# Optimization experiments

Hardware: AMD Instinct MI355X
Metric: run time of the kernel (lower is better)

The kernel has to match this reference:

```python
import jax, jax.numpy as jnp
import numpy as np

# ---- constants mirroring ATSSPostProcessor defaults / metainfo ----
PRE_NMS_THRESH = 0.05
PRE_NMS_TOP_N = 1000
NMS_THRESH = 0.6
POST_TOP_N = 100
IMG_H, IMG_W = 800.0, 1216.0      # metainfo img_shape
BW_XY, BW_WH = 10.0, 5.0          # GLIP/ATSS box coder weights (10,10,5,5)
MAX_DWH = float(np.log(1000.0 / 16.0))
CLASS_OFFSET = 10000.0            # batched_nms class offset (> max coord)


def setup_inputs() -> dict:
    key = jax.random.key(0)
    k0, k1, k2, k3 = jax.random.split(key, 4)
    N, C, L, H, W = 8, 80, 256, 100, 152
    box_regression = jax.random.normal(k0, (N, 4, H, W), jnp.float32)
    centerness = jax.random.normal(k1, (N, 1, H, W), jnp.float32)
    box_cls = jax.random.normal(k2, (N, C, H, W), jnp.float32)
    dot_product_logits = jax.random.normal(k3, (N, H * W, L), jnp.float32)
    # stride-8 grid anchors with base size 64
    ys, xs = np.meshgrid(np.arange(H), np.arange(W), indexing='ij')
    cx, cy = (xs + 0.5) * 8.0, (ys + 0.5) * 8.0
    anchors = jnp.asarray(
        np.stack([cx - 32, cy - 32, cx + 32, cy + 32], -1).reshape(-1, 4),
        jnp.float32)
    # MEAN aggregation positive map: class j <- tokens [3j, 3j+1, 3j+2]
    pm = np.zeros((C, L), np.float32)
    for j in range(C):
        pm[j, 3 * j:3 * j + 3] = 1.0 / 3.0
    pos_map = jnp.asarray(pm)
    return dict(box_regression=box_regression, centerness=centerness,
                box_cls=box_cls, dot_product_logits=dot_product_logits,
                anchors=anchors, pos_map=pos_map)


def _decode(a, r):
    # delta_xywh decode with weights (10,10,5,5), clamped to img_shape
    aw, ah = a[..., 2] - a[..., 0], a[..., 3] - a[..., 1]
    acx, acy = a[..., 0] + 0.5 * aw, a[..., 1] + 0.5 * ah
    dx, dy = r[..., 0] / BW_XY, r[..., 1] / BW_XY
    dw = jnp.minimum(r[..., 2] / BW_WH, MAX_DWH)
    dh = jnp.minimum(r[..., 3] / BW_WH, MAX_DWH)
    pcx, pcy = dx * aw + acx, dy * ah + acy
    pw, ph = jnp.exp(dw) * aw, jnp.exp(dh) * ah
    x1 = jnp.clip(pcx - 0.5 * pw, 0.0, IMG_W)
    y1 = jnp.clip(pcy - 0.5 * ph, 0.0, IMG_H)
    x2 = jnp.clip(pcx + 0.5 * pw, 0.0, IMG_W)
    y2 = jnp.clip(pcy + 0.5 * ph, 0.0, IMG_H)
    return jnp.stack([x1, y1, x2, y2], -1)


def _iou_matrix(b):  # b: [K,4]
    area = (b[:, 2] - b[:, 0]) * (b[:, 3] - b[:, 1])
    ix1 = jnp.maximum(b[:, None, 0], b[None, :, 0])
    iy1 = jnp.maximum(b[:, None, 1], b[None, :, 1])
    ix2 = jnp.minimum(b[:, None, 2], b[None, :, 2])
    iy2 = jnp.minimum(b[:, None, 3], b[None, :, 3])
    inter = jnp.maximum(ix2 - ix1, 0.0) * jnp.maximum(iy2 - iy1, 0.0)
    return inter / (area[:, None] + area[None, :] - inter + 1e-6)


def _nms_single(boxes, scores, labels, valid):
    # class-aware greedy NMS (batched_nms) on fixed-size K candidates
    K = boxes.shape[0]
    s = jnp.where(valid, scores, -1.0)
    order = jnp.argsort(-s)
    b, s, l, v = boxes[order], s[order], labels[order], valid[order]
    ob = b + (l.astype(b.dtype) * CLASS_OFFSET)[:, None]
    iou = _iou_matrix(ob)
    ar = jnp.arange(K)

    def body(i, keep):
        sup = keep[i] & (iou[i] > NMS_THRESH) & (ar > i)
        return keep & ~sup

    keep = jax.lax.fori_loop(0, K, body, v)
    s2 = jnp.where(keep, s, -1.0)
    topv, topi = jax.lax.top_k(s2, POST_TOP_N)
    good = topv > 0.0
    fb = jnp.where(good[:, None], b[topi], 0.0)
    fs = jnp.where(good, topv, 0.0)
    fl = jnp.where(good, l[topi], 0)
    return fb, fs, fl


def reference(box_regression, centerness, box_cls, dot_product_logits,
              anchors, pos_map):
    N = box_regression.shape[0]
    C = pos_map.shape[0]
    HW = anchors.shape[0]
    # permute_and_flatten: [N,4,H,W] -> [N,HW,4]
    reg = box_regression.transpose(0, 2, 3, 1).reshape(N, HW, 4)
    ctr = jax.nn.sigmoid(centerness.reshape(N, HW))
    # sigmoid score fusion + MEAN grounding->od aggregation
    dp = jax.nn.sigmoid(dot_product_logits)            # [N,HW,L]
    scores = jnp.einsum('nkl,cl->nkc', dp, pos_map)    # [N,HW,C]
    cand = scores > PRE_NMS_THRESH
    fused = scores * ctr[:, :, None]
    # dynamic per-image topk over candidates == fixed-K masked top_k
    masked = jnp.where(cand, fused, -1.0).reshape(N, HW * C)
    vals, idx = jax.lax.top_k(masked, PRE_NMS_TOP_N)   # [N,K]
    valid = jnp.take_along_axis(cand.reshape(N, -1), idx, axis=1)
    loc = idx // C
    labels = idx % C + 1
    a = anchors[loc]                                           # [N,K,4]
    r = jnp.take_along_axis(reg, loc[..., None], axis=1)       # [N,K,4]
    boxes = _decode(a, r)
    sc = jnp.sqrt(jnp.maximum(vals, 0.0))
    w = boxes[..., 2] - boxes[..., 0]
    h = boxes[..., 3] - boxes[..., 1]
    valid = valid & (w > 0) & (h > 0)  # min_size = 0 filter
    # scale_factor = 1.0 -> boxes unchanged
    out_boxes, out_scores, out_labels = jax.vmap(_nms_single)(
        boxes, sc, labels, valid)
    return out_boxes, out_scores, out_labels
```

## Files before the change

### kernel.cpp

```cpp
#include <hip/hip_runtime.h>
#include <hip/hip_bf16.h>

#define NIMG 8
#define NC   80
#define NL   256
#define HWQ  15200
#define TOPK 1000
#define CAP  4096
#define SSORT 2048
#define NPOST 100
#define PERIMG (HWQ * NC)
#define TOTAL (NIMG * PERIMG)
#define NROW 16
#define NBLK (NIMG * HWQ / NROW)
#define PI4  (PERIMG / 4)
#define WPI  (PI4 / 64)
#define NWAVE (NIMG * WPI)
#define CBLK (TOTAL / 4 / 256)

__device__ __forceinline__ unsigned flipKey(float f) {
    unsigned u = __float_as_uint(f);
    return u ^ (((unsigned)((int)u >> 31)) | 0x80000000u);
}
__device__ __forceinline__ float unflipKey(unsigned k) {
    unsigned u = k ^ ((k & 0x80000000u) ? 0x80000000u : 0xFFFFFFFFu);
    return __uint_as_float(u);
}
__device__ __forceinline__ float sigmoidf(float x) {
    return 1.0f / (1.0f + expf(-x));
}

__global__ void kprep(const float* __restrict__ pm, unsigned* nnz,
                      unsigned* tok, float* wt) {
    int c = blockIdx.x * blockDim.x + threadIdx.x;
    if (c >= NC) return;
    int cnt = 0;
    for (int l = 0; l < NL; ++l) {
        float v = pm[c * NL + l];
        if (v != 0.0f) { tok[cnt * NC + c] = l; wt[cnt * NC + c] = v; cnt++; }
    }
    nnz[c] = cnt;
}

__global__ void __launch_bounds__(256)
kscoreh(const float* __restrict__ dp, const float* __restrict__ cent,
        const unsigned* __restrict__ nnz, const unsigned* __restrict__ tok,
        const float* __restrict__ wt, float* __restrict__ scores,
        unsigned* __restrict__ gh) {
    __shared__ float srow[NROW * NL];
    __shared__ unsigned h[4096];
    int t = threadIdx.x;
    for (int i = t; i < 4096; i += 256) h[i] = 0;
    long long base = (long long)blockIdx.x * NROW;
    const float4* src = (const float4*)(dp + base * NL);
    float4* dst = (float4*)srow;
#pragma unroll
    for (int j = 0; j < 4; ++j) dst[t + j * 256] = src[t + j * 256];
    __syncthreads();
    long long obase = base * NC;
#pragma unroll
    for (int j = 0; j < 5; ++j) {
        int o = t + j * 256;
        int r = o / NC, c = o - r * NC;
        const float* row = srow + r * NL;
        int m = (int)nnz[c];
        float acc = 0.0f;
        if (m == 3) {
            int t0 = (int)tok[c], t1 = (int)tok[NC + c], t2 = (int)tok[2 * NC + c];
            float w0 = wt[c], w1 = wt[NC + c], w2 = wt[2 * NC + c];
            float s0 = sigmoidf(row[t0]);
            float s1 = sigmoidf(row[t1]);
            float s2 = sigmoidf(row[t2]);
            acc += s0 * w0; acc += s1 * w1; acc += s2 * w2;
        } else {
            for (int q = 0; q < m; ++q)
                acc += sigmoidf(row[tok[q * NC + c]]) * wt[q * NC + c];
        }
        float ctr = sigmoidf(cent[base + r]);
        float sc = (acc > 0.05f) ? acc * ctr : -1.0f;
        scores[obase + o] = sc;
        atomicAdd(&h[flipKey(sc) >> 20], 1u);
    }
    __syncthreads();
    int n = (int)(base / HWQ);
    for (int i = t; i < 4096; i += 256)
        if (h[i]) atomicAdd(&gh[n * 4096 + i], h[i]);
}

__global__ void kfind1(const unsigned* __restrict__ gh, unsigned* meta) {
    __shared__ unsigned h[4096];
    __shared__ unsigned psum[256];
    int n = blockIdx.x;
    for (int i = threadIdx.x; i < 4096; i += 256) h[i] = gh[n * 4096 + i];
    __syncthreads();
    unsigned s = 0;
    for (int i = 0; i < 16; ++i) s += h[threadIdx.x * 16 + i];
    psum[threadIdx.x] = s;
    __syncthreads();
    if (threadIdx.x == 0) {
        unsigned cum = 0, above = 0; int B = 0; bool done = false;
        for (int seg = 255; seg >= 0 && !done; --seg) {
            if (cum + psum[seg] >= TOPK) {
                for (int b = seg * 16 + 15; b >= seg * 16; --b) {
                    if (cum + h[b] >= TOPK) { B = b; above = cum; done = true; break; }
                    cum += h[b];
                }
            } else cum += psum[seg];
        }
        meta[n] = (unsigned)B;
        meta[8 + n] = above;
    }
}

__global__ void __launch_bounds__(256)
kcount(const float4* __restrict__ scores4, const unsigned* __restrict__ meta,
       unsigned* __restrict__ wavecnt) {
    int i4 = blockIdx.x * 256 + threadIdx.x;
    int n = i4 / PI4;
    unsigned B = meta[n];
    float4 v = scores4[i4];
    int ns = 0;
    ns += ((flipKey(v.x) >> 20) >= B);
    ns += ((flipKey(v.y) >> 20) >= B);
    ns += ((flipKey(v.z) >> 20) >= B);
    ns += ((flipKey(v.w) >> 20) >= B);
    int s = ns;
#pragma unroll
    for (int off = 1; off < 64; off <<= 1) s += __shfl_xor(s, off);
    if ((threadIdx.x & 63) == 0) wavecnt[i4 >> 6] = (unsigned)s;
}

__global__ void __launch_bounds__(1024)
kscan(const unsigned* __restrict__ wavecnt, unsigned* __restrict__ waveoff,
      unsigned* __restrict__ cnt) {
    __shared__ unsigned ps[1024];
    int n = blockIdx.x, t = threadIdx.x;
    const unsigned* wc = wavecnt + n * WPI;
    unsigned* wo = waveoff + n * WPI;
    int s0 = t * 5;
    unsigned loc[5]; unsigned sum = 0;
#pragma unroll
    for (int j = 0; j < 5; ++j) {
        int i = s0 + j;
        unsigned vv = (i < WPI) ? wc[i] : 0u;
        loc[j] = sum; sum += vv;
    }
    ps[t] = sum;
    __syncthreads();
    for (int off = 1; off < 1024; off <<= 1) {
        unsigned add = (t >= off) ? ps[t - off] : 0u;
        __syncthreads();
        ps[t] += add;
        __syncthreads();
    }
    unsigned excl = (t > 0) ? ps[t - 1] : 0u;
#pragma unroll
    for (int j = 0; j < 5; ++j) {
        int i = s0 + j;
        if (i < WPI) wo[i] = excl + loc[j];
    }
    if (t == 1023) cnt[n] = ps[1023];
}

__global__ void __launch_bounds__(256)
kwrite(const float4* __restrict__ scores4, const unsigned* __restrict__ meta,
       const unsigned* __restrict__ waveoff, unsigned long long* __restrict__ cand) {
    int i4 = blockIdx.x * 256 + threadIdx.x;
    int n = i4 / PI4;
    unsigned B = meta[n];
    float4 v = scores4[i4];
    int li0 = (i4 - n * PI4) * 4;
    unsigned keys[4]; int sel[4]; int ns = 0;
    keys[0] = flipKey(v.x); sel[0] = (keys[0] >> 20) >= B; ns += sel[0];
    keys[1] = flipKey(v.y); sel[1] = (keys[1] >> 20) >= B; ns += sel[1];
    keys[2] = flipKey(v.z); sel[2] = (keys[2] >> 20) >= B; ns += sel[2];
    keys[3] = flipKey(v.w); sel[3] = (keys[3] >> 20) >= B; ns += sel[3];
    int lane = threadIdx.x & 63;
    int pre = ns;
#pragma unroll
    for (int off = 1; off < 64; off <<= 1) {
        int o = __shfl_up(pre, off);
        if (lane >= off) pre += o;
    }
    unsigned base = waveoff[i4 >> 6] + (unsigned)(pre - ns);
    unsigned long long* cbase = cand + (size_t)n * CAP;
#pragma unroll
    for (int e = 0; e < 4; ++e) {
        if (sel[e]) {
            if (base < CAP)
                cbase[base] = ((unsigned long long)keys[e] << 32)
                              | (unsigned)(~(li0 + e));
            base++;
        }
    }
}

__global__ void __launch_bounds__(1024)
kfine(const unsigned long long* __restrict__ cand, const unsigned* __restrict__ cnt,
      const unsigned* __restrict__ meta, unsigned long long* __restrict__ sorted) {
    __shared__ unsigned h[4096];
    __shared__ unsigned long long sbuf[SSORT];
    __shared__ unsigned psum[256];
    __shared__ unsigned selcnt;
    __shared__ unsigned Fbin;
    int n = blockIdx.x, t = threadIdx.x;
    int M = min(cnt[n], (unsigned)CAP);
    unsigned B = meta[n], above = meta[8 + n];
    const unsigned long long* cb = cand + (size_t)n * CAP;
    for (int i = t; i < 4096; i += 1024) h[i] = 0;
    sbuf[t] = 0ULL; sbuf[t + 1024] = 0ULL;
    if (t == 0) selcnt = 0;
    __syncthreads();
    for (int i = t; i < M; i += 1024) {
        unsigned key = (unsigned)(cb[i] >> 32);
        if ((key >> 20) == B) atomicAdd(&h[(key >> 8) & 0xFFFu], 1u);
    }
    __syncthreads();
    if (t < 256) {
        unsigned s = 0;
        for (int i = 0; i < 16; ++i) s += h[t * 16 + i];
        psum[t] = s;
    }
    __syncthreads();
    if (t == 0) {
        unsigned cum = above; int F = 0; bool done = false;
        for (int seg = 255; seg >= 0 && !done; --seg) {
            if (cum + psum[seg] >= TOPK) {
                for (int b = seg * 16 + 15; b >= seg * 16; --b) {
                    if (cum + h[b] >= TOPK) { F = b; done = true; break; }
                    cum += h[b];
                }
            } else cum += psum[seg];
        }
        Fbin = (unsigned)F;
    }
    __syncthreads();
    unsigned T24 = (B << 12) | Fbin;
    for (int i = t; i < M; i += 1024) {
        unsigned long long e = cb[i];
        unsigned key = (unsigned)(e >> 32);
        if ((key >> 8) >= T24) {
            unsigned p = atomicAdd(&selcnt, 1u);
            if (p < SSORT) sbuf[p] = e;
        }
    }
    __syncthreads();
    int s = (int)selcnt;
    int SN = (s <= 1024) ? 1024 : SSORT;
    for (int k = 2; k <= SN; k <<= 1) {
        for (int j = k >> 1; j > 0; j >>= 1) {
            for (int i = t; i < SN; i += 1024) {
                int l = i ^ j;
                if (l > i) {
                    unsigned long long a = sbuf[i], b = sbuf[l];
                    bool sw = ((i & k) == 0) ? (a < b) : (a > b);
                    if (sw) { sbuf[i] = b; sbuf[l] = a; }
                }
            }
            __syncthreads();
        }
    }
    if (t < TOPK) sorted[(n << 10) + t] = sbuf[t];
}

__global__ void __launch_bounds__(256)
kdecode(const unsigned long long* __restrict__ sorted,
        const float* __restrict__ anchors, const float* __restrict__ breg,
        float4* __restrict__ box4, float4* __restrict__ obx4,
        float* __restrict__ areag, unsigned* __restrict__ lblkeep) {
    int gid = blockIdx.x * 256 + threadIdx.x;
    if (gid >= NIMG * TOPK) return;
    int n = gid / TOPK, r = gid - n * TOPK;
    int o = (n << 10) + r;
    unsigned long long e = sorted[o];
    unsigned key = (unsigned)(e >> 32);
    bool real = key > 0x80000000u;
    unsigned li = ~(unsigned)(e & 0xFFFFFFFFu);
    unsigned k = li / NC, c = li - k * NC;
    int label = (int)c + 1;
    float x1 = 0, y1 = 0, x2 = 0, y2 = 0;
    bool val = false;
    if (real) {
        float a0 = anchors[k * 4 + 0], a1 = anchors[k * 4 + 1];
        float a2 = anchors[k * 4 + 2], a3 = anchors[k * 4 + 3];
        float r0 = breg[(n * 4 + 0) * HWQ + k];
        float r1 = breg[(n * 4 + 1) * HWQ + k];
        float r2 = breg[(n * 4 + 2) * HWQ + k];
        float r3 = breg[(n * 4 + 3) * HWQ + k];
        float aw = a2 - a0, ah = a3 - a1;
        float acx = a0 + 0.5f * aw, acy = a1 + 0.5f * ah;
        float dx = r0 / 10.0f, dy = r1 / 10.0f;
        float dw = fminf(r2 / 5.0f, 4.135166556742356f);
        float dh = fminf(r3 / 5.0f, 4.135166556742356f);
        float pcx = dx * aw + acx, pcy = dy * ah + acy;
        float pw = expf(dw) * aw, ph = expf(dh) * ah;
        x1 = fminf(fmaxf(pcx - 0.5f * pw, 0.0f), 1216.0f);
        y1 = fminf(fmaxf(pcy - 0.5f * ph, 0.0f), 800.0f);
        x2 = fminf(fmaxf(pcx + 0.5f * pw, 0.0f), 1216.0f);
        y2 = fminf(fmaxf(pcy + 0.5f * ph, 0.0f), 800.0f);
        val = (x2 - x1 > 0.0f) && (y2 - y1 > 0.0f);
    }
    box4[o] = make_float4(x1, y1, x2, y2);
    float off = (float)label * 10000.0f;
    float o0 = x1 + off, o1 = y1 + off, o2 = x2 + off, o3 = y2 + off;
    obx4[o] = make_float4(o0, o1, o2, o3);
    areag[o] = (o2 - o0) * (o3 - o1);
    lblkeep[o] = (unsigned)(real ? label : 0) | ((val ? 1u : 0u) << 16);
}

__global__ void __launch_bounds__(1024)
knms2(const unsigned long long* __restrict__ sorted,
      const float4* __restrict__ obx4, const float* __restrict__ areag,
      const unsigned* __restrict__ lblkeep, const float4* __restrict__ box4,
      float* __restrict__ outBoxes, float* __restrict__ outScores,
      float* __restrict__ outLabels) {
    __shared__ float ob0[TOPK], ob1[TOPK], ob2[TOPK], ob3[TOPK], area[TOPK];
    __shared__ unsigned long long sup[TOPK];
    __shared__ unsigned short lbl[TOPK];
    __shared__ unsigned char  keepf[TOPK];
    __shared__ unsigned short wrank[TOPK];
    __shared__ unsigned short clist[TOPK];
    __shared__ unsigned short cstart[NC + 1];
    __shared__ unsigned ccnt[NC];
    __shared__ int pfx[1024];
    __shared__ int smax;

    int n = blockIdx.x, t = threadIdx.x;
    if (t < NC) ccnt[t] = 0;
    if (t == 0) smax = 0;
    if (t < TOPK) {
        int o = (n << 10) + t;
        float4 ob = obx4[o];
        ob0[t] = ob.x; ob1[t] = ob.y; ob2[t] = ob.z; ob3[t] = ob.w;
        area[t] = areag[o];
        unsigned lk = lblkeep[o];
        lbl[t] = (unsigned short)(lk & 0xFFFFu);
        keepf[t] = (unsigned char)(lk >> 16);
        sup[t] = 0ULL;
    }
    __syncthreads();

    if (t < TOPK) {
        unsigned short my = lbl[t];
        int w = 0;
        if (my) {
            for (int r = 0; r < t; ++r) w += (lbl[r] == my);
            atomicAdd(&ccnt[my - 1], 1u);
        }
        wrank[t] = (unsigned short)w;
    }
    __syncthreads();
    if (t < NC) atomicMax(&smax, (int)ccnt[t]);
    __syncthreads();
    if (t == 0) {
        unsigned s = 0;
        for (int c = 0; c < NC; ++c) { cstart[c] = (unsigned short)s; s += ccnt[c]; }
        cstart[NC] = (unsigned short)s;
    }
    __syncthreads();
    if (t < TOPK && lbl[t]) clist[cstart[lbl[t] - 1] + wrank[t]] = (unsigned short)t;
    __syncthreads();

    if (smax <= 64) {
        if (t < TOPK && lbl[t]) {
            int base = cstart[lbl[t] - 1];
            int w = wrank[t];
            float A0 = ob0[t], A1 = ob1[t], A2 = ob2[t], A3 = ob3[t], Aa = area[t];
            unsigned long long m = 0ULL;
            for (int j = 0; j < w; ++j) {
                int ib = clist[base + j];
                float iw = fminf(A2, ob2[ib]) - fmaxf(A0, ob0[ib]);
                float ih = fminf(A3, ob3[ib]) - fmaxf(A1, ob1[ib]);
                float inter = fmaxf(iw, 0.0f) * fmaxf(ih, 0.0f);
                float denom = Aa + area[ib] - inter + 1e-6f;
                if (inter / denom > 0.6f) m |= (1ull << j);
            }
            sup[t] = m;
        }
        __syncthreads();
        if (t < NC) {
            unsigned long long kb = 0ULL;
            int base = cstart[t], mc = (int)ccnt[t];
            for (int w = 0; w < mc; ++w) {
                int i = clist[base + w];
                bool kp = keepf[i] && ((sup[i] & kb) == 0ULL);
                keepf[i] = kp ? 1 : 0;
                if (kp) kb |= (1ull << w);
            }
        }
    } else {
        __syncthreads();
        if (t < NC) {
            int s0 = cstart[t], s1 = s0 + (int)ccnt[t];
            for (int a = s0; a < s1; ++a) {
                int ia = clist[a];
                if (!keepf[ia]) continue;
                float A0 = ob0[ia], A1 = ob1[ia], A2 = ob2[ia], A3 = ob3[ia];
                float Aa = area[ia];
                for (int b = a + 1; b < s1; ++b) {
                    int ib = clist[b];
                    if (!keepf[ib]) continue;
                    float iw = fminf(A2, ob2[ib]) - fmaxf(A0, ob0[ib]);
                    float ih = fminf(A3, ob3[ib]) - fmaxf(A1, ob1[ib]);
                    float inter = fmaxf(iw, 0.0f) * fmaxf(ih, 0.0f);
                    float denom = Aa + area[ib] - inter + 1e-6f;
                    if (inter / denom > 0.6f) keepf[ib] = 0;
                }
            }
        }
    }
    __syncthreads();

    pfx[t] = (t < TOPK) ? (int)keepf[t] : 0;
    __syncthreads();
    for (int off = 1; off < 1024; off <<= 1) {
        int add = (t >= off) ? pfx[t - off] : 0;
        __syncthreads();
        pfx[t] += add;
        __syncthreads();
    }
    int total = pfx[1023];

    if (t < TOPK && keepf[t]) {
        int q = pfx[t] - 1;
        if (q < NPOST) {
            int o = (n << 10) + t;
            float4 b = box4[o];
            float fused = unflipKey((unsigned)(sorted[o] >> 32));
            outBoxes[(n * NPOST + q) * 4 + 0] = b.x;
            outBoxes[(n * NPOST + q) * 4 + 1] = b.y;
            outBoxes[(n * NPOST + q) * 4 + 2] = b.z;
            outBoxes[(n * NPOST + q) * 4 + 3] = b.w;
            outScores[n * NPOST + q] = sqrtf(fmaxf(fused, 0.0f));
            outLabels[n * NPOST + q] = (float)lbl[t];
        }
    }
    if (t < NPOST && t >= total) {
        outBoxes[(n * NPOST + t) * 4 + 0] = 0.0f;
        outBoxes[(n * NPOST + t) * 4 + 1] = 0.0f;
        outBoxes[(n * NPOST + t) * 4 + 2] = 0.0f;
        outBoxes[(n * NPOST + t) * 4 + 3] = 0.0f;
        outScores[n * NPOST + t] = 0.0f;
        outLabels[n * NPOST + t] = 0.0f;
    }
}

extern "C" void kernel_launch(void* const* d_in, const int* in_sizes, int n_in,
                              void* d_out, int out_size, void* d_ws, size_t ws_size,
                              hipStream_t stream) {
    const float* breg = (const float*)d_in[0];
    const float* cent = (const float*)d_in[1];
    const float* dp   = (const float*)d_in[3];
    const float* anc  = (const float*)d_in[4];
    const float* pm   = (const float*)d_in[5];

    char* ws = (char*)d_ws;
    size_t off_scores  = 0;
    size_t off_gh      = off_scores + (size_t)TOTAL * 4;
    size_t off_cnt     = off_gh + (size_t)NIMG * 4096 * 4;
    size_t off_meta    = off_cnt + 128;
    size_t off_cand    = off_meta + 128;
    size_t off_wavecnt = off_cand + (size_t)NIMG * CAP * 8;
    size_t off_waveoff = off_wavecnt + (size_t)NWAVE * 4 + 64;
    size_t off_nnz     = off_waveoff + (size_t)NWAVE * 4 + 64;
    size_t off_tok     = off_nnz + 512;
    size_t off_wt      = off_tok + (size_t)NC * NL * 4;
    size_t needed      = off_wt + (size_t)NC * NL * 4;
    if (ws_size < needed) return;

    size_t off_sorted = off_scores;
    size_t off_box4   = off_sorted + (size_t)NIMG * 1024 * 8;
    size_t off_obx4   = off_box4 + (size_t)NIMG * 1024 * 16;
    size_t off_area   = off_obx4 + (size_t)NIMG * 1024 * 16;
    size_t off_lblk   = off_area + (size_t)NIMG * 1024 * 4;

    float*    scores  = (float*)(ws + off_scores);
    unsigned* gh      = (unsigned*)(ws + off_gh);
    unsigned* cnt     = (unsigned*)(ws + off_cnt);
    unsigned* meta    = (unsigned*)(ws + off_meta);
    unsigned long long* cand = (unsigned long long*)(ws + off_cand);
    unsigned* wavecnt = (unsigned*)(ws + off_wavecnt);
    unsigned* waveoff = (unsigned*)(ws + off_waveoff);
    unsigned* nnz     = (unsigned*)(ws + off_nnz);
    unsigned* tok     = (unsigned*)(ws + off_tok);
    float*    wt      = (float*)(ws + off_wt);
    unsigned long long* sorted = (unsigned long long*)(ws + off_sorted);
    float4*   box4    = (float4*)(ws + off_box4);
    float4*   obx4    = (float4*)(ws + off_obx4);
    float*    areag   = (float*)(ws + off_area);
    unsigned* lblkeep = (unsigned*)(ws + off_lblk);

    hipMemsetAsync(ws + off_gh, 0, (size_t)NIMG * 4096 * 4, stream);

    kprep<<<1, 128, 0, stream>>>(pm, nnz, tok, wt);
    kscoreh<<<NBLK, 256, 0, stream>>>(dp, cent, nnz, tok, wt, scores, gh);
    kfind1<<<NIMG, 256, 0, stream>>>(gh, meta);
    kcount<<<CBLK, 256, 0, stream>>>((const float4*)scores, meta, wavecnt);
    kscan<<<NIMG, 1024, 0, stream>>>(wavecnt, waveoff, cnt);
    kwrite<<<CBLK, 256, 0, stream>>>((const float4*)scores, meta, waveoff, cand);
    kfine<<<NIMG, 1024, 0, stream>>>(cand, cnt, meta, sorted);
    kdecode<<<(NIMG * TOPK + 255) / 256, 256, 0, stream>>>(sorted, anc, breg,
                                                           box4, obx4, areag, lblkeep);

    float* outBoxes  = (float*)d_out;
    float* outScores = outBoxes + NIMG * NPOST * 4;
    float* outLabels = outScores + NIMG * NPOST;
    knms2<<<NIMG, 1024, 0, stream>>>(sorted, obx4, areag, lblkeep, box4,
                                     outBoxes, outScores, outLabels);
}
```

Measured before the change: 216.4 us.

## Replace count/scan compaction with per-wave atomic append; skip LDS staging of logits

Removes the kcount and kscan kernels. kwrite now reserves output slots with one atomicAdd per wave on a per-image counter, which the memset now zeroes, so the 39 MB score buffer is read once instead of twice and two launches go away. In kscoreh, the 16 logit rows are no longer staged into shared memory; only the three needed tokens per class are read straight from global memory, and the centerness sigmoid is computed once per row. The tradeoff is that candidate order becomes nondeterministic, which relies on the later fine sort being order-independent, and the direct gathers may use full cache lines less efficiently.

```diff
diff --git a/kernel.cpp b/kernel.cpp
--- a/kernel.cpp
+++ b/kernel.cpp
@@ -14,8 +14,6 @@
 #define NROW 16
 #define NBLK (NIMG * HWQ / NROW)
 #define PI4  (PERIMG / 4)
-#define WPI  (PI4 / 64)
-#define NWAVE (NIMG * WPI)
 #define CBLK (TOTAL / 4 / 256)
 
 __device__ __forceinline__ unsigned flipKey(float f) {
@@ -47,22 +45,20 @@
         const unsigned* __restrict__ nnz, const unsigned* __restrict__ tok,
         const float* __restrict__ wt, float* __restrict__ scores,
         unsigned* __restrict__ gh) {
-    __shared__ float srow[NROW * NL];
     __shared__ unsigned h[4096];
+    __shared__ float sctr[NROW];
     int t = threadIdx.x;
     for (int i = t; i < 4096; i += 256) h[i] = 0;
     long long base = (long long)blockIdx.x * NROW;
-    const float4* src = (const float4*)(dp + base * NL);
-    float4* dst = (float4*)srow;
-#pragma unroll
-    for (int j = 0; j < 4; ++j) dst[t + j * 256] = src[t + j * 256];
+    if (t < NROW) sctr[t] = sigmoidf(cent[base + t]);
     __syncthreads();
     long long obase = base * NC;
+    const float* dpb = dp + base * NL;
 #pragma unroll
     for (int j = 0; j < 5; ++j) {
         int o = t + j * 256;
         int r = o / NC, c = o - r * NC;
-        const float* row = srow + r * NL;
+        const float* row = dpb + r * NL;
         int m = (int)nnz[c];
         float acc = 0.0f;
         if (m == 3) {
@@ -76,8 +72,7 @@
             for (int q = 0; q < m; ++q)
                 acc += sigmoidf(row[tok[q * NC + c]]) * wt[q * NC + c];
         }
-        float ctr = sigmoidf(cent[base + r]);
-        float sc = (acc > 0.05f) ? acc * ctr : -1.0f;
+        float sc = (acc > 0.05f) ? acc * sctr[r] : -1.0f;
         scores[obase + o] = sc;
         atomicAdd(&h[flipKey(sc) >> 20], 1u);
     }
@@ -113,58 +108,8 @@
 }
 
 __global__ void __launch_bounds__(256)
-kcount(const float4* __restrict__ scores4, const unsigned* __restrict__ meta,
-       unsigned* __restrict__ wavecnt) {
-    int i4 = blockIdx.x * 256 + threadIdx.x;
-    int n = i4 / PI4;
-    unsigned B = meta[n];
-    float4 v = scores4[i4];
-    int ns = 0;
-    ns += ((flipKey(v.x) >> 20) >= B);
-    ns += ((flipKey(v.y) >> 20) >= B);
-    ns += ((flipKey(v.z) >> 20) >= B);
-    ns += ((flipKey(v.w) >> 20) >= B);
-    int s = ns;
-#pragma unroll
-    for (int off = 1; off < 64; off <<= 1) s += __shfl_xor(s, off);
-    if ((threadIdx.x & 63) == 0) wavecnt[i4 >> 6] = (unsigned)s;
-}
-
-__global__ void __launch_bounds__(1024)
-kscan(const unsigned* __restrict__ wavecnt, unsigned* __restrict__ waveoff,
-      unsigned* __restrict__ cnt) {
-    __shared__ unsigned ps[1024];
-    int n = blockIdx.x, t = threadIdx.x;
-    const unsigned* wc = wavecnt + n * WPI;
-    unsigned* wo = waveoff + n * WPI;
-    int s0 = t * 5;
-    unsigned loc[5]; unsigned sum = 0;
-#pragma unroll
-    for (int j = 0; j < 5; ++j) {
-        int i = s0 + j;
-        unsigned vv = (i < WPI) ? wc[i] : 0u;
-        loc[j] = sum; sum += vv;
-    }
-    ps[t] = sum;
-    __syncthreads();
-    for (int off = 1; off < 1024; off <<= 1) {
-        unsigned add = (t >= off) ? ps[t - off] : 0u;
-        __syncthreads();
-        ps[t] += add;
-        __syncthreads();
-    }
-    unsigned excl = (t > 0) ? ps[t - 1] : 0u;
-#pragma unroll
-    for (int j = 0; j < 5; ++j) {
-        int i = s0 + j;
-        if (i < WPI) wo[i] = excl + loc[j];
-    }
-    if (t == 1023) cnt[n] = ps[1023];
-}
-
-__global__ void __launch_bounds__(256)
 kwrite(const float4* __restrict__ scores4, const unsigned* __restrict__ meta,
-       const unsigned* __restrict__ waveoff, unsigned long long* __restrict__ cand) {
+       unsigned* __restrict__ cnt, unsigned long long* __restrict__ cand) {
     int i4 = blockIdx.x * 256 + threadIdx.x;
     int n = i4 / PI4;
     unsigned B = meta[n];
@@ -182,7 +127,13 @@
         int o = __shfl_up(pre, off);
         if (lane >= off) pre += o;
     }
-    unsigned base = waveoff[i4 >> 6] + (unsigned)(pre - ns);
+    int wtot = __shfl(pre, 63);
+    unsigned wbase = 0;
+    if (wtot) {
+        if (lane == 63) wbase = atomicAdd(&cnt[n], (unsigned)wtot);
+        wbase = (unsigned)__shfl((int)wbase, 63);
+    }
+    unsigned base = wbase + (unsigned)(pre - ns);
     unsigned long long* cbase = cand + (size_t)n * CAP;
 #pragma unroll
     for (int e = 0; e < 4; ++e) {
@@ -460,9 +411,7 @@
     size_t off_cnt     = off_gh + (size_t)NIMG * 4096 * 4;
     size_t off_meta    = off_cnt + 128;
     size_t off_cand    = off_meta + 128;
-    size_t off_wavecnt = off_cand + (size_t)NIMG * CAP * 8;
-    size_t off_waveoff = off_wavecnt + (size_t)NWAVE * 4 + 64;
-    size_t off_nnz     = off_waveoff + (size_t)NWAVE * 4 + 64;
+    size_t off_nnz     = off_cand + (size_t)NIMG * CAP * 8;
     size_t off_tok     = off_nnz + 512;
     size_t off_wt      = off_tok + (size_t)NC * NL * 4;
     size_t needed      = off_wt + (size_t)NC * NL * 4;
@@ -479,8 +428,6 @@
     unsigned* cnt     = (unsigned*)(ws + off_cnt);
     unsigned* meta    = (unsigned*)(ws + off_meta);
     unsigned long long* cand = (unsigned long long*)(ws + off_cand);
-    unsigned* wavecnt = (unsigned*)(ws + off_wavecnt);
-    unsigned* waveoff = (unsigned*)(ws + off_waveoff);
     unsigned* nnz     = (unsigned*)(ws + off_nnz);
     unsigned* tok     = (unsigned*)(ws + off_tok);
     float*    wt      = (float*)(ws + off_wt);
@@ -490,14 +437,12 @@
     float*    areag   = (float*)(ws + off_area);
     unsigned* lblkeep = (unsigned*)(ws + off_lblk);
 
-    hipMemsetAsync(ws + off_gh, 0, (size_t)NIMG * 4096 * 4, stream);
+    hipMemsetAsync(ws + off_gh, 0, (size_t)NIMG * 4096 * 4 + 128, stream);
 
     kprep<<<1, 128, 0, stream>>>(pm, nnz, tok, wt);
     kscoreh<<<NBLK, 256, 0, stream>>>(dp, cent, nnz, tok, wt, scores, gh);
     kfind1<<<NIMG, 256, 0, stream>>>(gh, meta);
-    kcount<<<CBLK, 256, 0, stream>>>((const float4*)scores, meta, wavecnt);
-    kscan<<<NIMG, 1024, 0, stream>>>(wavecnt, waveoff, cnt);
-    kwrite<<<CBLK, 256, 0, stream>>>((const float4*)scores, meta, waveoff, cand);
+    kwrite<<<CBLK, 256, 0, stream>>>((const float4*)scores, meta, cnt, cand);
     kfine<<<NIMG, 1024, 0, stream>>>(cand, cnt, meta, sorted);
     kdecode<<<(NIMG * TOPK + 255) / 256, 256, 0, stream>>>(sorted, anc, breg,
                                                            box4, obx4, areag, lblkeep);
```

Result: slower. 294.5 us (+36.1%).
